# Performance work log

Measured on AMD Instinct MI355X. Metric: run time of the kernel, lower is better.

Reference implementation:

```python
import jax, jax.numpy as jnp
import numpy as np

B, L, D = 4, 2048, 1024
E, F, H = 6, 1536, 512  # experts, d_ff, router hidden
TOP_K = 2
LN_EPS = 1e-5

def setup_inputs() -> dict:
    key = jax.random.key(0)
    ks = jax.random.split(key, 8)
    s = lambda fan: 1.0 / np.sqrt(fan)
    return {
        "x": jax.random.normal(ks[0], (B, L, D), jnp.float32),
        "r1_w": jax.random.normal(ks[1], (D, H), jnp.float32) * s(D),
        "r1_b": jnp.zeros((H,), jnp.float32),
        "ln_g": jnp.ones((H,), jnp.float32),
        "ln_b": jnp.zeros((H,), jnp.float32),
        "r2_w": jax.random.normal(ks[2], (H, E), jnp.float32) * s(H),
        "r2_b": jnp.zeros((E,), jnp.float32),
        "temp": jnp.ones((1,), jnp.float32),
        "route_bias": jnp.zeros((E,), jnp.float32),
        "W1": jax.random.normal(ks[3], (E, D, F), jnp.float32) * s(D),
        "b1": jnp.zeros((E, F), jnp.float32),
        "W2": jax.random.normal(ks[4], (E, F, D), jnp.float32) * s(F),
        "b2": jnp.zeros((E, D), jnp.float32),
    }

def reference(x, r1_w, r1_b, ln_g, ln_b, r2_w, r2_b, temp, route_bias, W1, b1, W2, b2):
    b, l, d = x.shape
    xf = x.reshape(-1, d)                       # [N, D]
    n = xf.shape[0]
    # Router: Linear -> LayerNorm -> GELU(exact) -> Linear
    h = xf @ r1_w + r1_b                        # [N, H]
    mu = jnp.mean(h, axis=-1, keepdims=True)
    var = jnp.mean((h - mu) ** 2, axis=-1, keepdims=True)
    h = (h - mu) * jax.lax.rsqrt(var + LN_EPS) * ln_g + ln_b
    h = jax.nn.gelu(h, approximate=False)
    logits = (h @ r2_w + r2_b) / temp + route_bias   # [N, E]
    p = jax.nn.softmax(logits, axis=-1)
    top_v, top_i = jax.lax.top_k(p, TOP_K)      # [N, k]
    probs = jnp.zeros_like(p).at[jnp.arange(n)[:, None], top_i].set(top_v)  # [N, E]
    # Dense all-expert MLPs (faithful to source, which computes every expert)
    hh = jnp.einsum('nd,edf->enf', xf, W1) + b1[:, None, :]   # [E, N, F]
    even = (jnp.arange(W1.shape[0]) % 2 == 0)[:, None, None]
    act = jnp.where(even, jax.nn.gelu(hh, approximate=False), jax.nn.silu(hh))
    eo = jnp.einsum('enf,efd->end', act, W2) + b2[:, None, :]  # [E, N, D]
    out = jnp.einsum('ne,end->nd', probs, eo)   # weighted combine
    return out.reshape(b, l, d)
```

## Files before the change

### kernel.cpp

```cpp
#include <hip/hip_runtime.h>
#include <hip/hip_bf16.h>
#include <stdint.h>

typedef __bf16 bf16;
typedef bf16 bf16x8 __attribute__((ext_vector_type(8)));
typedef bf16 bf16x4 __attribute__((ext_vector_type(4)));
typedef float f32x4 __attribute__((ext_vector_type(4)));
typedef int i32x4 __attribute__((ext_vector_type(4)));

#define N_TOK 8192
#define D_MODEL 1024
#define H_R 512
#define N_EXP 6
#define F_FF 1536
#define FLAG_CAP 1024
#define PMAX 17

__device__ __forceinline__ float erf_fast(float x) {
    float ax = fabsf(x);
    float t = 1.0f / (1.0f + 0.3275911f * ax);
    float p = t * (0.254829592f + t * (-0.284496736f + t * (1.421413741f +
              t * (-1.453152027f + t * 1.061405429f))));
    float r = 1.0f - p * __expf(-ax * ax);
    return copysignf(r, x);
}
__device__ __forceinline__ float gelu_f(float x) {
    return 0.5f * x * (1.0f + erf_fast(x * 0.70710678118654752f));
}
__device__ __forceinline__ float silu_f(float x) {
    return x * (1.0f / (1.0f + __expf(-x)));
}

typedef __attribute__((address_space(1))) const void* gas1;
typedef __attribute__((address_space(3))) void* las3;

__device__ __forceinline__ void gload16(const void* g, void* l) {
    __builtin_amdgcn_global_load_lds((gas1)g, (las3)l, 16, 0, 0);
}

__device__ __forceinline__ int swz_src_q(int c) {
    return (((c & 3) - ((c >> 2) >> 1)) & 3);
}

#define GATE(N) asm volatile("s_waitcnt vmcnt(" #N ")\n\ts_barrier" ::: "memory")


__global__ __launch_bounds__(256) void convert_x_split(
    const float* __restrict__ x, bf16* __restrict__ xh, bf16* __restrict__ xl) {
    size_t i = ((size_t)blockIdx.x * 256 + threadIdx.x) * 8;
    f32x4 a = *(const f32x4*)(x + i);
    f32x4 b = *(const f32x4*)(x + i + 4);
    float v[8] = {a[0], a[1], a[2], a[3], b[0], b[1], b[2], b[3]};
    bf16x8 vh, vl;
    #pragma unroll
    for (int k = 0; k < 8; ++k) {
        bf16 h = (bf16)v[k];
        vh[k] = h;
        vl[k] = (bf16)(v[k] - (float)h);
    }
    *(bf16x8*)(xh + i) = vh;
    *(bf16x8*)(xl + i) = vl;
}

__global__ __launch_bounds__(256) void transpose_bf16_64(
    const float* __restrict__ in, bf16* __restrict__ out, int R, int C) {
    __shared__ float tile[64][65];
    const float* inp = in + (size_t)blockIdx.z * R * C;
    bf16* op = out + (size_t)blockIdx.z * R * C;
    int tx = threadIdx.x & 15, ty = threadIdx.x >> 4;
    int r0 = blockIdx.y * 64, c0 = blockIdx.x * 64;
    #pragma unroll
    for (int p = 0; p < 4; ++p) {
        int row = p * 16 + ty;
        f32x4 v = *(const f32x4*)(inp + (size_t)(r0 + row) * C + c0 + tx * 4);
        tile[row][tx * 4 + 0] = v[0];
        tile[row][tx * 4 + 1] = v[1];
        tile[row][tx * 4 + 2] = v[2];
        tile[row][tx * 4 + 3] = v[3];
    }
    __syncthreads();
    #pragma unroll
    for (int p = 0; p < 4; ++p) {
        int cc = p * 16 + ty;
        bf16x4 o;
        #pragma unroll
        for (int k = 0; k < 4; ++k) o[k] = (bf16)tile[tx * 4 + k][cc];
        *(bf16x4*)(op + (size_t)(c0 + cc) * R + r0 + tx * 4) = o;
    }
}

__global__ __launch_bounds__(256) void transpose_split(
    const float* __restrict__ in, bf16* __restrict__ oh, bf16* __restrict__ ol,
    int R, int C) {
    __shared__ float tile[32][33];
    int tx = threadIdx.x & 31, ty = threadIdx.x >> 5;
    int r0 = blockIdx.y * 32, c0 = blockIdx.x * 32;
    #pragma unroll
    for (int yy = ty; yy < 32; yy += 8)
        tile[yy][tx] = in[(size_t)(r0 + yy) * C + c0 + tx];
    __syncthreads();
    #pragma unroll
    for (int yy = ty; yy < 32; yy += 8) {
        float v = tile[tx][yy];
        bf16 h = (bf16)v;
        size_t o = (size_t)(c0 + yy) * R + r0 + tx;
        oh[o] = h;
        ol[o] = (bf16)(v - (float)h);
    }
}


__device__ __forceinline__ void gemm128_core(
    const bf16* gA0, const bf16* gA1, const bf16* gB0, const bf16* gB1,
    int K, bf16* sm, f32x4 acc[4][4])
{
    const int tid = threadIdx.x;
    const int lane = tid & 63;
    const int w = tid >> 6;
    const int wm = w & 1, wn = w >> 1;
    const int lc = lane & 15;
    const int koff = ((((lane >> 4) + (lc >> 1)) & 3) * 8);
    const int ws = w * 512;
    const int NT = K >> 5;
    gload16(gA0,      sm + ws);
    gload16(gA1,      sm + 2048 + ws);
    gload16(gB0,      sm + 4096 + ws);
    gload16(gB1,      sm + 6144 + ws);
    gload16(gA0 + 32, sm + 8192 + ws);
    gload16(gA1 + 32, sm + 8192 + 2048 + ws);
    gload16(gB0 + 32, sm + 8192 + 4096 + ws);
    gload16(gB1 + 32, sm + 8192 + 6144 + ws);
    int cur = 0, nxt = 8192, fut = 16384;
    for (int t = 0; t < NT; ++t) {
        if (t + 2 < NT) {
            const int kb = (t + 2) << 5;
            gload16(gA0 + kb, sm + fut + ws);
            gload16(gA1 + kb, sm + fut + 2048 + ws);
            gload16(gB0 + kb, sm + fut + 4096 + ws);
            gload16(gB1 + kb, sm + fut + 6144 + ws);
            GATE(8);
        } else if (t + 1 < NT) {
            GATE(4);
        } else {
            GATE(0);
        }
        bf16x8 af[4], bfr[4];
        #pragma unroll
        for (int i = 0; i < 4; ++i)
            af[i] = *(const bf16x8*)(sm + cur + (wm * 64 + i * 16 + lc) * 32 + koff);
        #pragma unroll
        for (int j = 0; j < 4; ++j)
            bfr[j] = *(const bf16x8*)(sm + cur + 4096 + (wn * 64 + j * 16 + lc) * 32 + koff);
        __builtin_amdgcn_s_barrier();
        __builtin_amdgcn_s_setprio(1);
        #pragma unroll
        for (int i = 0; i < 4; ++i)
            #pragma unroll
            for (int j = 0; j < 4; ++j)
                acc[i][j] = __builtin_amdgcn_mfma_f32_16x16x32_bf16(af[i], bfr[j], acc[i][j], 0, 0, 0);
        __builtin_amdgcn_s_setprio(0);
        int old = cur; cur = nxt; nxt = fut; fut = old;
    }
}


__global__ __launch_bounds__(256, 2) void router_gemm_fused(
    const bf16* __restrict__ xh, const bf16* __restrict__ xl,
    const bf16* __restrict__ wTh, const bf16* __restrict__ wTl,
    float* __restrict__ hp) {
    __shared__ bf16 smem[32768];
    const int tid = threadIdx.x;
    const int mbase = blockIdx.y * 128, nbase = blockIdx.x * 128;
    const int c0 = tid, c1 = tid + 256;
    const size_t ra0 = (size_t)(mbase + (c0 >> 2)) * D_MODEL + swz_src_q(c0) * 8;
    const size_t ra1 = (size_t)(mbase + (c1 >> 2)) * D_MODEL + swz_src_q(c1) * 8;
    const size_t rb0 = (size_t)(nbase + (c0 >> 2)) * D_MODEL + swz_src_q(c0) * 8;
    const size_t rb1 = (size_t)(nbase + (c1 >> 2)) * D_MODEL + swz_src_q(c1) * 8;
    const bf16 *pxh0 = xh + ra0, *pxh1 = xh + ra1;
    const bf16 *pxl0 = xl + ra0, *pxl1 = xl + ra1;
    const bf16 *pwh0 = wTh + rb0, *pwh1 = wTh + rb1;
    const bf16 *pwl0 = wTl + rb0, *pwl1 = wTl + rb1;
    const int w = tid >> 6, lane = tid & 63;
    const int wm = w & 1, wn = w >> 1, lc = lane & 15;
    const int koff = ((((lane >> 4) + (lc >> 1)) & 3) * 8);
    const int ws = w * 512;
    f32x4 acc[4][4] = {};
    gload16(pxh0, smem + ws);
    gload16(pxh1, smem + 2048 + ws);
    gload16(pxl0, smem + 4096 + ws);
    gload16(pxl1, smem + 6144 + ws);
    gload16(pwh0, smem + 8192 + ws);
    gload16(pwh1, smem + 10240 + ws);
    gload16(pwl0, smem + 12288 + ws);
    gload16(pwl1, smem + 14336 + ws);
    int bo = 0;
    for (int t = 0; t < D_MODEL / 32; ++t) {
        const int nb = bo ^ 16384;
        if (t + 1 < D_MODEL / 32) {
            const int kb = (t + 1) << 5;
            gload16(pxh0 + kb, smem + nb + ws);
            gload16(pxh1 + kb, smem + nb + 2048 + ws);
            gload16(pxl0 + kb, smem + nb + 4096 + ws);
            gload16(pxl1 + kb, smem + nb + 6144 + ws);
            gload16(pwh0 + kb, smem + nb + 8192 + ws);
            gload16(pwh1 + kb, smem + nb + 10240 + ws);
            gload16(pwl0 + kb, smem + nb + 12288 + ws);
            gload16(pwl1 + kb, smem + nb + 14336 + ws);
            GATE(8);
        } else {
            GATE(0);
        }
        bf16x8 ah[4], al[4], bh[4], bl[4];
        #pragma unroll
        for (int i = 0; i < 4; ++i) {
            const int ro = (wm * 64 + i * 16 + lc) * 32 + koff;
            ah[i] = *(const bf16x8*)(smem + bo + ro);
            al[i] = *(const bf16x8*)(smem + bo + 4096 + ro);
        }
        #pragma unroll
        for (int j = 0; j < 4; ++j) {
            const int ro = (wn * 64 + j * 16 + lc) * 32 + koff;
            bh[j] = *(const bf16x8*)(smem + bo + 8192 + ro);
            bl[j] = *(const bf16x8*)(smem + bo + 12288 + ro);
        }
        __builtin_amdgcn_s_barrier();
        __builtin_amdgcn_s_setprio(1);
        #pragma unroll
        for (int i = 0; i < 4; ++i)
            #pragma unroll
            for (int j = 0; j < 4; ++j) {
                acc[i][j] = __builtin_amdgcn_mfma_f32_16x16x32_bf16(ah[i], bh[j], acc[i][j], 0, 0, 0);
                acc[i][j] = __builtin_amdgcn_mfma_f32_16x16x32_bf16(ah[i], bl[j], acc[i][j], 0, 0, 0);
                acc[i][j] = __builtin_amdgcn_mfma_f32_16x16x32_bf16(al[i], bh[j], acc[i][j], 0, 0, 0);
            }
        __builtin_amdgcn_s_setprio(0);
        bo = nb;
    }
    const int quad = lane >> 4;
    #pragma unroll
    for (int i = 0; i < 4; ++i)
        #pragma unroll
        for (int j = 0; j < 4; ++j) {
            int col = nbase + wn * 64 + j * 16 + lc;
            #pragma unroll
            for (int r = 0; r < 4; ++r) {
                int row = mbase + wm * 64 + i * 16 + quad * 4 + r;
                hp[(size_t)row * H_R + col] = acc[i][j][r];
            }
        }
}


__global__ __launch_bounds__(256) void ln_router2(
    const float* __restrict__ hp, const float* __restrict__ r1b,
    const float* __restrict__ g, const float* __restrict__ bta,
    const float* __restrict__ r2w, const float* __restrict__ r2b,
    const float* __restrict__ temp, const float* __restrict__ rbias,
    int* __restrict__ top_i, float* __restrict__ top_p,
    int* __restrict__ flaglist, int* __restrict__ meta) {
    __shared__ float Wl[H_R * N_EXP];
    int tid = threadIdx.x;
    for (int i = tid; i < H_R * N_EXP; i += 256) Wl[i] = r2w[i];
    __syncthreads();
    int w = tid >> 6, lane = tid & 63;
    int t = blockIdx.x * 4 + w;
    size_t rbase = (size_t)t * H_R;
    int k0 = lane * 8;
    float v[8];
    {
        f32x4 a0 = *(const f32x4*)(hp + rbase + k0);
        f32x4 a1 = *(const f32x4*)(hp + rbase + k0 + 4);
        f32x4 d0 = *(const f32x4*)(r1b + k0);
        f32x4 d1 = *(const f32x4*)(r1b + k0 + 4);
        #pragma unroll
        for (int k = 0; k < 4; ++k) {
            v[k]     = a0[k] + d0[k];
            v[k + 4] = a1[k] + d1[k];
        }
    }
    float s = 0.f;
    #pragma unroll
    for (int k = 0; k < 8; ++k) s += v[k];
    #pragma unroll
    for (int off = 32; off; off >>= 1) s += __shfl_xor(s, off);
    float mu = s * (1.0f / H_R);
    float q = 0.f;
    #pragma unroll
    for (int k = 0; k < 8; ++k) { float d = v[k] - mu; q += d * d; }
    #pragma unroll
    for (int off = 32; off; off >>= 1) q += __shfl_xor(q, off);
    float scl = 1.0f / sqrtf(q * (1.0f / H_R) + 1e-5f);
    f32x4 g0 = *(const f32x4*)(g + k0), g1 = *(const f32x4*)(g + k0 + 4);
    f32x4 b0 = *(const f32x4*)(bta + k0), b1v = *(const f32x4*)(bta + k0 + 4);
    float G[8] = {g0[0], g0[1], g0[2], g0[3], g1[0], g1[1], g1[2], g1[3]};
    float B[8] = {b0[0], b0[1], b0[2], b0[3], b1v[0], b1v[1], b1v[2], b1v[3]};
    float acc[N_EXP] = {};
    #pragma unroll
    for (int k = 0; k < 8; ++k) {
        float y = gelu_f((v[k] - mu) * scl * G[k] + B[k]);
        const float* wr = &Wl[(k0 + k) * N_EXP];
        #pragma unroll
        for (int e = 0; e < N_EXP; ++e) acc[e] += y * wr[e];
    }
    #pragma unroll
    for (int e = 0; e < N_EXP; ++e)
        #pragma unroll
        for (int off = 32; off; off >>= 1) acc[e] += __shfl_xor(acc[e], off);
    if (lane == 0) {
        float tinv = 1.0f / temp[0];
        float lg[N_EXP];
        #pragma unroll
        for (int e = 0; e < N_EXP; ++e) lg[e] = (acc[e] + r2b[e]) * tinv + rbias[e];
        float v1 = -1e30f; int i1 = 0;
        #pragma unroll
        for (int e = 0; e < N_EXP; ++e) if (lg[e] > v1) { v1 = lg[e]; i1 = e; }
        float v2 = -1e30f; int i2 = 0;
        #pragma unroll
        for (int e = 0; e < N_EXP; ++e) if (e != i1 && lg[e] > v2) { v2 = lg[e]; i2 = e; }
        float v3 = -1e30f;
        #pragma unroll
        for (int e = 0; e < N_EXP; ++e) if (e != i1 && e != i2 && lg[e] > v3) v3 = lg[e];
        float ssum = 0.f;
        #pragma unroll
        for (int e = 0; e < N_EXP; ++e) ssum += __expf(lg[e] - v1);
        float inv = 1.0f / ssum;
        top_i[2 * t] = i1; top_i[2 * t + 1] = i2;
        top_p[2 * t] = inv;
        top_p[2 * t + 1] = __expf(v2 - v1) * inv;
        if (v2 - v3 < 1e-3f) {
            int ix = atomicAdd(&meta[24], 1);
            if (ix < FLAG_CAP) flaglist[ix] = t;
        }
    }
}


__global__ __launch_bounds__(256) void router_rescue(
    const float* __restrict__ x, const float* __restrict__ r1w,
    const float* __restrict__ r1b, const float* __restrict__ lng,
    const float* __restrict__ lnb, const float* __restrict__ r2w,
    const float* __restrict__ r2b, const float* __restrict__ temp,
    const float* __restrict__ rbias, const int* __restrict__ flaglist,
    const int* __restrict__ meta, int* __restrict__ top_i, float* __restrict__ top_p) {
    int n = meta[24]; if (n > FLAG_CAP) n = FLAG_CAP;
    if ((int)blockIdx.x >= n) return;
    int t = flaglist[blockIdx.x];
    __shared__ double xs[D_MODEL];
    __shared__ double hbuf[H_R];
    __shared__ double red[8];
    int tid = threadIdx.x;
    for (int k = tid; k < D_MODEL; k += 256) xs[k] = (double)x[(size_t)t * D_MODEL + k];
    __syncthreads();
    for (int c = tid; c < H_R; c += 256) {
        double s = 0.0;
        for (int k = 0; k < D_MODEL; ++k) s += xs[k] * (double)r1w[(size_t)k * H_R + c];
        hbuf[c] = s + (double)r1b[c];
    }
    __syncthreads();
    double ls = 0.0;
    for (int c = tid; c < H_R; c += 256) ls += hbuf[c];
    #pragma unroll
    for (int off = 32; off; off >>= 1) ls += __shfl_xor(ls, off);
    if ((tid & 63) == 0) red[tid >> 6] = ls;
    __syncthreads();
    double mu = (red[0] + red[1] + red[2] + red[3]) * (1.0 / H_R);
    __syncthreads();
    double q = 0.0;
    for (int c = tid; c < H_R; c += 256) { double d = hbuf[c] - mu; q += d * d; }
    #pragma unroll
    for (int off = 32; off; off >>= 1) q += __shfl_xor(q, off);
    if ((tid & 63) == 0) red[tid >> 6] = q;
    __syncthreads();
    double var = (red[0] + red[1] + red[2] + red[3]) * (1.0 / H_R);
    double scl = 1.0 / sqrt(var + 1e-5);
    __syncthreads();
    for (int c = tid; c < H_R; c += 256) {
        double y = (hbuf[c] - mu) * scl * (double)lng[c] + (double)lnb[c];
        hbuf[c] = 0.5 * y * (1.0 + erf(y * 0.70710678118654752440));
    }
    __syncthreads();
    if (tid < N_EXP) {
        double s = 0.0;
        for (int k = 0; k < H_R; ++k) s += hbuf[k] * (double)r2w[k * N_EXP + tid];
        red[tid] = (s + (double)r2b[tid]) / (double)temp[0] + (double)rbias[tid];
    }
    __syncthreads();
    if (tid == 0) {
        double lg[N_EXP];
        #pragma unroll
        for (int e = 0; e < N_EXP; ++e) lg[e] = red[e];
        double v1 = -1e300; int i1 = 0;
        for (int e = 0; e < N_EXP; ++e) if (lg[e] > v1) { v1 = lg[e]; i1 = e; }
        double v2 = -1e300; int i2 = 0;
        for (int e = 0; e < N_EXP; ++e) if (e != i1 && lg[e] > v2) { v2 = lg[e]; i2 = e; }
        double s = 0.0;
        for (int e = 0; e < N_EXP; ++e) s += exp(lg[e] - v1);
        double inv = 1.0 / s;
        top_i[2 * t] = i1; top_i[2 * t + 1] = i2;
        top_p[2 * t] = (float)inv;
        top_p[2 * t + 1] = (float)(exp(v2 - v1) * inv);
    }
}


#define RP_T 1024
#define RP_TOK (N_TOK / RP_T)

__global__ __launch_bounds__(1024) void route_pack(
    const int* __restrict__ top_i, const float* __restrict__ top_p,
    int* __restrict__ meta, int* __restrict__ atok, float* __restrict__ pw,
    int* __restrict__ ptab) {
    __shared__ int S[N_EXP][RP_T];
    __shared__ int segbase[N_EXP + 1];
    int tid = threadIdx.x;
    int e_loc[2 * RP_TOK];
    int cnt[N_EXP];
    #pragma unroll
    for (int e = 0; e < N_EXP; ++e) cnt[e] = 0;
    int t0 = tid * RP_TOK;
    #pragma unroll
    for (int q = 0; q < (2 * RP_TOK) / 4; ++q) {
        i32x4 v = *(const i32x4*)(top_i + 2 * t0 + q * 4);
        #pragma unroll
        for (int k = 0; k < 4; ++k) {
            int e = v[k];
            e_loc[q * 4 + k] = e;
            #pragma unroll
            for (int ee = 0; ee < N_EXP; ++ee) if (e == ee) cnt[ee]++;
        }
    }
    #pragma unroll
    for (int e = 0; e < N_EXP; ++e) S[e][tid] = cnt[e];
    __syncthreads();
    for (int off = 1; off < RP_T; off <<= 1) {
        int tmp[N_EXP];
        #pragma unroll
        for (int e = 0; e < N_EXP; ++e)
            tmp[e] = (tid >= off) ? S[e][tid - off] : 0;
        __syncthreads();
        #pragma unroll
        for (int e = 0; e < N_EXP; ++e) S[e][tid] += tmp[e];
        __syncthreads();
    }
    if (tid == 0) {
        int o = 0;
        int tp = 0;
        #pragma unroll
        for (int e = 0; e < N_EXP; ++e) {
            segbase[e] = o;
            int tot = S[e][RP_T - 1];
            meta[e] = tot;
            meta[8 + e] = o;
            o += tot;
            int np = (tot + 127) >> 7;
            for (int y = 0; y < np; ++y) ptab[tp++] = e | (y << 8);
        }
        segbase[N_EXP] = o;
        meta[16] = tp;
    }
    __syncthreads();
    int pos[N_EXP];
    #pragma unroll
    for (int e = 0; e < N_EXP; ++e)
        pos[e] = segbase[e] + S[e][tid] - cnt[e];
    #pragma unroll
    for (int k = 0; k < 2 * RP_TOK; ++k) {
        int e = e_loc[k];
        int a = 0;
        #pragma unroll
        for (int ee = 0; ee < N_EXP; ++ee) if (e == ee) a = pos[ee]++;
        atok[a] = t0 + (k >> 1);
        pw[a] = top_p[2 * t0 + k];
    }
}


#define NX1 (F_FF / 128)
#define NX2 (D_MODEL / 128)

__global__ __launch_bounds__(256, 3) void expert_gemm1(
    const bf16* __restrict__ xb, const bf16* __restrict__ W1T,
    const float* __restrict__ b1, const int* __restrict__ meta,
    const int* __restrict__ atok, const int* __restrict__ ptab,
    bf16* __restrict__ act) {
    __shared__ bf16 smem[24576];
    const int id = blockIdx.x;
    const int xcd = id & 7, slot = id >> 3;
    const int p = slot / NX1, xt = slot % NX1;
    const int total = meta[16];
    const int Q = (total + 7) >> 3;
    const int gidx = xcd * Q + p;
    if (p >= Q || gidx >= total) return;
    const int ent = ptab[gidx];
    const int e = ent & 255, y = ent >> 8;
    int rows = meta[e];
    int mloc = y * 128;
    int base = meta[8 + e];
    int tid = threadIdx.x;
    int nbase = xt * 128;
    int c0 = tid, c1 = tid + 256;
    int r0 = mloc + (c0 >> 2); if (r0 > rows - 1) r0 = rows - 1;
    int r1 = mloc + (c1 >> 2); if (r1 > rows - 1) r1 = rows - 1;
    const bf16* gA0 = xb + (size_t)atok[base + r0] * D_MODEL + swz_src_q(c0) * 8;
    const bf16* gA1 = xb + (size_t)atok[base + r1] * D_MODEL + swz_src_q(c1) * 8;
    const bf16* Bt = W1T + ((size_t)e * F_FF + nbase) * D_MODEL;
    const bf16* gB0 = Bt + (size_t)(c0 >> 2) * D_MODEL + swz_src_q(c0) * 8;
    const bf16* gB1 = Bt + (size_t)(c1 >> 2) * D_MODEL + swz_src_q(c1) * 8;
    f32x4 acc[4][4] = {};
    gemm128_core(gA0, gA1, gB0, gB1, D_MODEL, smem, acc);
    const int lane = tid & 63;
    const int w = tid >> 6;
    const int wm = w & 1, wn = w >> 1;
    const int lc = lane & 15, qd = lane >> 4;
    const bool oddE = (e & 1) != 0;
    #pragma unroll
    for (int i = 0; i < 4; ++i) {
        #pragma unroll
        for (int j = 0; j < 4; ++j) {
            int col = nbase + wn * 64 + j * 16 + lc;
            float bias = b1[e * F_FF + col];
            #pragma unroll
            for (int r = 0; r < 4; ++r) {
                int rloc = mloc + wm * 64 + i * 16 + qd * 4 + r;
                if (rloc < rows) {
                    float vv = acc[i][j][r] + bias;
                    vv = oddE ? silu_f(vv) : gelu_f(vv);
                    act[(size_t)(base + rloc) * F_FF + col] = (bf16)vv;
                }
            }
        }
    }
}

__global__ __launch_bounds__(256, 3) void expert_gemm2(
    const bf16* __restrict__ act, const bf16* __restrict__ W2T,
    const float* __restrict__ b2, const int* __restrict__ meta,
    const int* __restrict__ atok, const float* __restrict__ pw,
    const int* __restrict__ ptab, float* __restrict__ out) {
    __shared__ bf16 smem[24576];
    const int id = blockIdx.x;
    const int xcd = id & 7, slot = id >> 3;
    const int p = slot / NX2, xt = slot % NX2;
    const int total = meta[16];
    const int Q = (total + 7) >> 3;
    const int gidx = xcd * Q + p;
    if (p >= Q || gidx >= total) return;
    const int ent = ptab[gidx];
    const int e = ent & 255, y = ent >> 8;
    int rows = meta[e];
    int mloc = y * 128;
    int base = meta[8 + e];
    int tid = threadIdx.x;
    int nbase = xt * 128;
    int c0 = tid, c1 = tid + 256;
    int r0 = mloc + (c0 >> 2); if (r0 > rows - 1) r0 = rows - 1;
    int r1 = mloc + (c1 >> 2); if (r1 > rows - 1) r1 = rows - 1;
    const bf16* gA0 = act + (size_t)(base + r0) * F_FF + swz_src_q(c0) * 8;
    const bf16* gA1 = act + (size_t)(base + r1) * F_FF + swz_src_q(c1) * 8;
    const bf16* Bt = W2T + ((size_t)e * D_MODEL + nbase) * F_FF;
    const bf16* gB0 = Bt + (size_t)(c0 >> 2) * F_FF + swz_src_q(c0) * 8;
    const bf16* gB1 = Bt + (size_t)(c1 >> 2) * F_FF + swz_src_q(c1) * 8;
    f32x4 acc[4][4] = {};
    gemm128_core(gA0, gA1, gB0, gB1, F_FF, smem, acc);
    const int lane = tid & 63;
    const int w = tid >> 6;
    const int wm = w & 1, wn = w >> 1;
    const int lc = lane & 15, qd = lane >> 4;
    #pragma unroll
    for (int i = 0; i < 4; ++i) {
        #pragma unroll
        for (int r = 0; r < 4; ++r) {
            int rloc = mloc + wm * 64 + i * 16 + qd * 4 + r;
            if (rloc < rows) {
                int token = atok[base + rloc];
                float wgt = pw[base + rloc];
                float* orow = out + (size_t)token * D_MODEL;
                #pragma unroll
                for (int j = 0; j < 4; ++j) {
                    int col = nbase + wn * 64 + j * 16 + lc;
                    atomicAdd(orow + col, wgt * (acc[i][j][r] + b2[e * D_MODEL + col]));
                }
            }
        }
    }
}


extern "C" void kernel_launch(void* const* d_in, const int* in_sizes, int n_in,
                              void* d_out, int out_size, void* d_ws, size_t ws_size,
                              hipStream_t stream) {
    const float* x     = (const float*)d_in[0];
    const float* r1w   = (const float*)d_in[1];
    const float* r1b   = (const float*)d_in[2];
    const float* lng   = (const float*)d_in[3];
    const float* lnb   = (const float*)d_in[4];
    const float* r2w   = (const float*)d_in[5];
    const float* r2b   = (const float*)d_in[6];
    const float* temp  = (const float*)d_in[7];
    const float* rbias = (const float*)d_in[8];
    const float* W1    = (const float*)d_in[9];
    const float* b1    = (const float*)d_in[10];
    const float* W2    = (const float*)d_in[11];
    const float* b2    = (const float*)d_in[12];
    float* out = (float*)d_out;

    char* ws = (char*)d_ws;
    size_t off = 0;
    auto alloc = [&](size_t bytes) -> void* {
        void* p = ws + off;
        off = (off + bytes + 255) & ~(size_t)255;
        return p;
    };
    bf16*  xh    = (bf16*)alloc((size_t)N_TOK * D_MODEL * 2);
    bf16*  xl    = (bf16*)alloc((size_t)N_TOK * D_MODEL * 2);
    bf16*  r1wTh = (bf16*)alloc((size_t)H_R * D_MODEL * 2);
    bf16*  r1wTl = (bf16*)alloc((size_t)H_R * D_MODEL * 2);
    bf16*  W1T   = (bf16*)alloc((size_t)N_EXP * F_FF * D_MODEL * 2);
    bf16*  W2T   = (bf16*)alloc((size_t)N_EXP * D_MODEL * F_FF * 2);
    float* hp    = (float*)alloc((size_t)N_TOK * H_R * 4);
    int*   top_i = (int*)alloc((size_t)N_TOK * 2 * 4);
    float* top_p = (float*)alloc((size_t)N_TOK * 2 * 4);
    int*   meta  = (int*)alloc(256);
    int*   flags = (int*)alloc(FLAG_CAP * 4);
    int*   atok  = (int*)alloc((size_t)2 * N_TOK * 4);
    float* pw    = (float*)alloc((size_t)2 * N_TOK * 4);
    int*   ptab  = (int*)alloc(1024);
    bf16*  actb  = (bf16*)alloc((size_t)2 * N_TOK * F_FF * 2);
    (void)ws_size; (void)n_in; (void)in_sizes;

    hipMemsetAsync(meta, 0, 256, stream);
    hipMemsetAsync(out, 0, (size_t)N_TOK * D_MODEL * 4, stream);

    convert_x_split<<<(N_TOK * D_MODEL) / (256 * 8), 256, 0, stream>>>(x, xh, xl);
    transpose_split<<<dim3(H_R / 32, D_MODEL / 32, 1), 256, 0, stream>>>(
        r1w, r1wTh, r1wTl, D_MODEL, H_R);

    router_gemm_fused<<<dim3(H_R / 128, N_TOK / 128, 1), 256, 0, stream>>>(
        xh, xl, r1wTh, r1wTl, hp);
    ln_router2<<<N_TOK / 4, 256, 0, stream>>>(
        hp, r1b, lng, lnb, r2w, r2b, temp, rbias, top_i, top_p, flags, meta);
    router_rescue<<<FLAG_CAP, 256, 0, stream>>>(
        x, r1w, r1b, lng, lnb, r2w, r2b, temp, rbias, flags, meta, top_i, top_p);
    route_pack<<<1, RP_T, 0, stream>>>(top_i, top_p, meta, atok, pw, ptab);

    transpose_bf16_64<<<dim3(F_FF / 64, D_MODEL / 64, N_EXP), 256, 0, stream>>>(
        W1, W1T, D_MODEL, F_FF);
    transpose_bf16_64<<<dim3(D_MODEL / 64, F_FF / 64, N_EXP), 256, 0, stream>>>(
        W2, W2T, F_FF, D_MODEL);

    expert_gemm1<<<8 * PMAX * NX1, 256, 0, stream>>>(
        xh, W1T, b1, meta, atok, ptab, actb);
    expert_gemm2<<<8 * PMAX * NX2, 256, 0, stream>>>(
        actb, W2T, b2, meta, atok, pw, ptab, out);
}
```

Baseline: 551.0 us.

## Replace atomic scatter-add in expert GEMM2 with buffered outputs and combine kernel

Expert GEMM2 now writes its unweighted per-slot outputs (plus bias) to an fp32 buffer instead of atomically adding weighted results into the output. A new combine kernel gathers each token's two expert rows through an inverse-permutation table and writes the weighted sum directly. This also drops the memset of the output. The aim is to avoid the cost of scattered global atomics, at the price of an extra 64MB write and read plus one more kernel launch.

```diff
diff --git a/kernel.cpp b/kernel.cpp
--- a/kernel.cpp
+++ b/kernel.cpp
@@ -407,9 +407,8 @@
 #define RP_TOK (N_TOK / RP_T)
 
 __global__ __launch_bounds__(1024) void route_pack(
-    const int* __restrict__ top_i, const float* __restrict__ top_p,
-    int* __restrict__ meta, int* __restrict__ atok, float* __restrict__ pw,
-    int* __restrict__ ptab) {
+    const int* __restrict__ top_i, int* __restrict__ meta,
+    int* __restrict__ atok, int* __restrict__ ainv, int* __restrict__ ptab) {
     __shared__ int S[N_EXP][RP_T];
     __shared__ int segbase[N_EXP + 1];
     int tid = threadIdx.x;
@@ -470,7 +469,7 @@
         #pragma unroll
         for (int ee = 0; ee < N_EXP; ++ee) if (e == ee) a = pos[ee]++;
         atok[a] = t0 + (k >> 1);
-        pw[a] = top_p[2 * t0 + k];
+        ainv[2 * t0 + k] = a;
     }
 }
 
@@ -535,8 +534,7 @@
 __global__ __launch_bounds__(256, 3) void expert_gemm2(
     const bf16* __restrict__ act, const bf16* __restrict__ W2T,
     const float* __restrict__ b2, const int* __restrict__ meta,
-    const int* __restrict__ atok, const float* __restrict__ pw,
-    const int* __restrict__ ptab, float* __restrict__ out) {
+    const int* __restrict__ ptab, float* __restrict__ eo) {
     __shared__ bf16 smem[24576];
     const int id = blockIdx.x;
     const int xcd = id & 7, slot = id >> 3;
@@ -569,20 +567,33 @@
     #pragma unroll
     for (int i = 0; i < 4; ++i) {
         #pragma unroll
-        for (int r = 0; r < 4; ++r) {
-            int rloc = mloc + wm * 64 + i * 16 + qd * 4 + r;
-            if (rloc < rows) {
-                int token = atok[base + rloc];
-                float wgt = pw[base + rloc];
-                float* orow = out + (size_t)token * D_MODEL;
-                #pragma unroll
-                for (int j = 0; j < 4; ++j) {
-                    int col = nbase + wn * 64 + j * 16 + lc;
-                    atomicAdd(orow + col, wgt * (acc[i][j][r] + b2[e * D_MODEL + col]));
-                }
+        for (int j = 0; j < 4; ++j) {
+            int col = nbase + wn * 64 + j * 16 + lc;
+            float bias = b2[e * D_MODEL + col];
+            #pragma unroll
+            for (int r = 0; r < 4; ++r) {
+                int rloc = mloc + wm * 64 + i * 16 + qd * 4 + r;
+                if (rloc < rows)
+                    eo[(size_t)(base + rloc) * D_MODEL + col] = acc[i][j][r] + bias;
             }
         }
     }
+}
+
+
+__global__ __launch_bounds__(256) void combine_kernel(
+    const float* __restrict__ eo, const int* __restrict__ ainv,
+    const float* __restrict__ top_p, float* __restrict__ out) {
+    int t = blockIdx.x;
+    int s0 = ainv[2 * t], s1 = ainv[2 * t + 1];
+    float p0 = top_p[2 * t], p1 = top_p[2 * t + 1];
+    int c = threadIdx.x * 4;
+    f32x4 a = *(const f32x4*)(eo + (size_t)s0 * D_MODEL + c);
+    f32x4 b = *(const f32x4*)(eo + (size_t)s1 * D_MODEL + c);
+    f32x4 o;
+    #pragma unroll
+    for (int k = 0; k < 4; ++k) o[k] = a[k] * p0 + b[k] * p1;
+    *(f32x4*)(out + (size_t)t * D_MODEL + c) = o;
 }
 
 
@@ -623,13 +634,13 @@
     int*   meta  = (int*)alloc(256);
     int*   flags = (int*)alloc(FLAG_CAP * 4);
     int*   atok  = (int*)alloc((size_t)2 * N_TOK * 4);
-    float* pw    = (float*)alloc((size_t)2 * N_TOK * 4);
+    int*   ainv  = (int*)alloc((size_t)2 * N_TOK * 4);
     int*   ptab  = (int*)alloc(1024);
     bf16*  actb  = (bf16*)alloc((size_t)2 * N_TOK * F_FF * 2);
+    float* eo    = (float*)alloc((size_t)2 * N_TOK * D_MODEL * 4);
     (void)ws_size; (void)n_in; (void)in_sizes;
 
     hipMemsetAsync(meta, 0, 256, stream);
-    hipMemsetAsync(out, 0, (size_t)N_TOK * D_MODEL * 4, stream);
 
     convert_x_split<<<(N_TOK * D_MODEL) / (256 * 8), 256, 0, stream>>>(x, xh, xl);
     transpose_split<<<dim3(H_R / 32, D_MODEL / 32, 1), 256, 0, stream>>>(
@@ -641,7 +652,7 @@
         hp, r1b, lng, lnb, r2w, r2b, temp, rbias, top_i, top_p, flags, meta);
     router_rescue<<<FLAG_CAP, 256, 0, stream>>>(
         x, r1w, r1b, lng, lnb, r2w, r2b, temp, rbias, flags, meta, top_i, top_p);
-    route_pack<<<1, RP_T, 0, stream>>>(top_i, top_p, meta, atok, pw, ptab);
+    route_pack<<<1, RP_T, 0, stream>>>(top_i, meta, atok, ainv, ptab);
 
     transpose_bf16_64<<<dim3(F_FF / 64, D_MODEL / 64, N_EXP), 256, 0, stream>>>(
         W1, W1T, D_MODEL, F_FF);
@@ -651,5 +662,6 @@
     expert_gemm1<<<8 * PMAX * NX1, 256, 0, stream>>>(
         xh, W1T, b1, meta, atok, ptab, actb);
     expert_gemm2<<<8 * PMAX * NX2, 256, 0, stream>>>(
-        actb, W2T, b2, meta, atok, pw, ptab, out);
-}
+        actb, W2T, b2, meta, ptab, eo);
+    combine_kernel<<<N_TOK, 256, 0, stream>>>(eo, ainv, top_p, out);
+}
```

Measured after the change: 532.3 us. 3.4% less time.
